# Performance work log

Hardware: AMD Instinct MI355X
Metric: run time of the kernel (lower is better)

The kernel has to match this reference:

```python
import jax, jax.numpy as jnp
import numpy as np
import math

B, C, BINS, W = 2, 8, 1024, 512
HEADS = 16
HD = BINS // HEADS          # 64 head dim
ROT = BINS // HEADS // 2    # 32 rotated dims
EXP = 4
EPS = 1e-5
MAX_FREQ = 10.0


def setup_inputs() -> dict:
    key = jax.random.key(0)
    ks = jax.random.split(key, 8)
    def u(k, shape, fan_in):
        lim = 1.0 / math.sqrt(fan_in)
        return jax.random.uniform(k, shape, jnp.float32, -lim, lim)
    return {
        "x": jax.random.normal(ks[0], (B, C, BINS, W), jnp.float32),
        "norm1_w": jnp.ones((BINS,), jnp.float32),
        "norm1_b": jnp.zeros((BINS,), jnp.float32),
        # 'pixel' rotary init: linspace(1, max_freq/2, dim//2) * pi (learned)
        "rot_freqs": jnp.linspace(1.0, MAX_FREQ / 2, ROT // 2, dtype=jnp.float32) * math.pi,
        "q_w": u(ks[1], (C, BINS, BINS), BINS),
        "out_w": u(ks[2], (C, BINS, BINS), BINS),
        "norm2_w": jnp.ones((BINS,), jnp.float32),
        "norm2_b": jnp.zeros((BINS,), jnp.float32),
        "lin1_w": u(ks[3], (C, BINS * EXP, BINS), BINS),
        "lin2_w": u(ks[4], (C, BINS, BINS * EXP), BINS * EXP),
    }


def _mlin(x, w):
    # x: [b,c,f_in,w]; w: [c,f_out,f_in] -> [b,c,f_out,w]
    return jnp.einsum('bcfw,cgf->bcgw', x, w)


def _frame_norm(x, w, b):
    # LayerNorm over the bins axis (axis=2) of [b,c,bins,w]
    m = jnp.mean(x, axis=2, keepdims=True)
    v = jnp.var(x, axis=2, keepdims=True)
    xn = (x - m) * jax.lax.rsqrt(v + EPS)
    return xn * w[:, None] + b[:, None]


def _rotate(q, cos, sin):
    # q: [b,c,h,w,d]; rotate first ROT dims with interleaved-pair rotate_half
    q1, q2 = q[..., :ROT], q[..., ROT:]
    qp = q1.reshape(*q1.shape[:-1], ROT // 2, 2)
    rh = jnp.stack([-qp[..., 1], qp[..., 0]], axis=-1).reshape(q1.shape)
    return jnp.concatenate([q1 * cos + rh * sin, q2], axis=-1)


def _attention(x, rot_freqs, q_w, out_w):
    b, c, bins, w = x.shape
    # faithful to source: q, k, v ALL use q_proj
    y = _mlin(x, q_w)  # [b,c,bins,w]
    # -> [b,c,h,w,d]
    y = y.transpose(0, 1, 3, 2).reshape(b, c, w, HEADS, HD).transpose(0, 1, 3, 2, 4)
    # rotary angles: t * freqs, repeat-interleaved x2 -> [w, ROT]
    t = jnp.arange(w, dtype=jnp.float32)
    ang = jnp.repeat(t[:, None] * rot_freqs[None, :], 2, axis=-1)
    cos, sin = jnp.cos(ang), jnp.sin(ang)
    q = _rotate(y, cos, sin)
    k = _rotate(y, cos, sin)
    v = y
    # NOTE: source scales by 1/sqrt(h) where h == bins (spectral height)
    scores = jnp.einsum('bchwd,bchud->bchwu', q, k) / math.sqrt(bins)
    a = jnp.einsum('bchwu,bchud->bchwd', jax.nn.softmax(scores, axis=-1), v)
    # [b,c,h,w,d] -> [b,c,bins,w]
    a = a.transpose(0, 1, 3, 2, 4).reshape(b, c, w, bins).transpose(0, 1, 3, 2)
    return _mlin(a, out_w)


def reference(x, norm1_w, norm1_b, rot_freqs, q_w, out_w,
              norm2_w, norm2_b, lin1_w, lin2_w):
    z = _frame_norm(x, norm1_w, norm1_b)
    z = _attention(z, rot_freqs, q_w, out_w)
    x = x + z  # dropout=0 -> identity
    z = _frame_norm(x, norm2_w, norm2_b)
    z = _mlin(jax.nn.gelu(_mlin(z, lin1_w), approximate=False), lin2_w)
    return x + z
```

## Files before the change

### kernel.cpp

```cpp
#include <hip/hip_runtime.h>
#include <math.h>

#define BB 2
#define CCH 8
#define BINS 1024
#define WW 512
#define HEADS 16
#define HD 64
#define ROTD 32
#define EXPF 4
#define NXE 8388608L
#define NTW 32

typedef unsigned short ushortT;
typedef short bf16x8 __attribute__((ext_vector_type(8)));
typedef float f32x4 __attribute__((ext_vector_type(4)));

__device__ __forceinline__ ushortT f2bf(float f) {
    unsigned int u = __float_as_uint(f);
    u = (u + 0x7FFF + ((u >> 16) & 1)) >> 16;
    return (ushortT)u;
}
__device__ __forceinline__ float bf2f(ushortT h) {
    return __uint_as_float(((unsigned int)h) << 16);
}
__device__ __forceinline__ float geluf(float x) {
    return 0.5f * x * (1.f + erff(x * 0.70710678118654752f));
}
__device__ __forceinline__ void gl_lds16(const ushortT* g, ushortT* l) {
    __builtin_amdgcn_global_load_lds(
        (const __attribute__((address_space(1))) unsigned int*)g,
        (__attribute__((address_space(3))) unsigned int*)l, 16, 0, 0);
}

__global__ __launch_bounds__(256)
void wcast_k(const float* __restrict__ s, ushortT* __restrict__ d, long n)
{
    long i = ((long)blockIdx.x * 256 + threadIdx.x) * 8;
    if (i >= n) return;
    float4 a = *(const float4*)&s[i];
    float4 b = *(const float4*)&s[i + 4];
    union { ushortT h[8]; uint4 v; } r;
    r.h[0] = f2bf(a.x); r.h[1] = f2bf(a.y); r.h[2] = f2bf(a.z); r.h[3] = f2bf(a.w);
    r.h[4] = f2bf(b.x); r.h[5] = f2bf(b.y); r.h[6] = f2bf(b.z); r.h[7] = f2bf(b.w);
    *(uint4*)&d[i] = r.v;
}

__global__ __launch_bounds__(1024)
void normT_k(const float* __restrict__ X, const float* __restrict__ wgt,
             const float* __restrict__ bia, ushortT* __restrict__ YT)
{
    __shared__ float tile[NTW][BINS + 1];
    __shared__ float red0[32][NTW], red1[32][NTW];
    __shared__ float ms[NTW], is[NTW];
    const int bc = blockIdx.x >> 4;
    const int w0 = (blockIdx.x & 15) * NTW;
    const int tid = threadIdx.x;
    const int w  = tid & (NTW - 1);
    const int fy = tid >> 5;
    const float* Xb = X + (long)bc * BINS * WW + w0;
    float s = 0.f, s2 = 0.f;
    for (int f = fy; f < BINS; f += 32) {
        float v = Xb[(long)f * WW + w];
        s += v; s2 += v * v;
        tile[w][f] = v;
    }
    red0[fy][w] = s; red1[fy][w] = s2;
    __syncthreads();
    if (tid < NTW) {
        float ss = 0.f, qq = 0.f;
        #pragma unroll
        for (int j = 0; j < 32; ++j) { ss += red0[j][tid]; qq += red1[j][tid]; }
        float m = ss * (1.f / BINS);
        float var = qq * (1.f / BINS) - m * m;
        ms[tid] = m; is[tid] = rsqrtf(var + 1e-5f);
    }
    __syncthreads();
    const int w2 = tid >> 5;
    const int c  = tid & 31;
    float m = ms[w2], inv = is[w2];
    ushortT* Yb = YT + ((long)bc * WW + w0 + w2) * BINS;
    #pragma unroll
    for (int jj = 0; jj < 4; ++jj) {
        int f0 = jj * 256 + c * 8;
        union { ushortT h[8]; uint4 v; } r;
        #pragma unroll
        for (int e = 0; e < 8; ++e) {
            int f = f0 + e;
            float v = (tile[w2][f] - m) * inv * wgt[f] + bia[f];
            r.h[e] = f2bf(v);
        }
        *(uint4*)&Yb[f0] = r.v;
    }
}

__global__ void rope_tab_k(const float* __restrict__ freqs,
                           float* __restrict__ cosT, float* __restrict__ sinT)
{
    int idx = blockIdx.x * 256 + threadIdx.x;
    if (idx >= WW * 16) return;
    int w = idx >> 4, i = idx & 15;
    float ang = (float)w * freqs[i];
    cosT[idx] = cosf(ang);
    sinT[idx] = sinf(ang);
}

__global__ __launch_bounds__(256)
void ropeB_k(const ushortT* __restrict__ yT, const float* __restrict__ cosT,
             const float* __restrict__ sinT, ushortT* __restrict__ rotT)
{
    long e0 = ((long)blockIdx.x * 256 + threadIdx.x) * 8;
    if (e0 >= NXE) return;
    int g0 = (int)(e0 & 1023);
    int w  = (int)((e0 >> 10) & 511);
    int d0 = g0 & 63;
    union { uint4 v; ushortT h8[8]; } in, ov;
    in.v = *(const uint4*)&yT[e0];
    if (d0 >= ROTD) {
        *(uint4*)&rotT[e0] = in.v;
        return;
    }
    #pragma unroll
    for (int j = 0; j < 8; j += 2) {
        int i = (d0 + j) >> 1;
        float c = cosT[w * 16 + i], s = sinT[w * 16 + i];
        float a = bf2f(in.h8[j]), b = bf2f(in.h8[j + 1]);
        ov.h8[j]     = f2bf(a * c - b * s);
        ov.h8[j + 1] = f2bf(b * c + a * s);
    }
    *(uint4*)&rotT[e0] = ov.v;
}

__global__ __launch_bounds__(256)
void mattn_k(const ushortT* __restrict__ rotT, const ushortT* __restrict__ yT,
             ushortT* __restrict__ oT)
{
    __shared__ ushortT Qs[64 * 64];
    __shared__ ushortT Ks[64 * 64];
    __shared__ ushortT Vs[64 * 72];
    __shared__ ushortT Ps[64 * 72];
    const int z = blockIdx.y;
    const int bc = z >> 4, h = z & 15;
    const int wq0 = blockIdx.x * 64;
    const int tid = threadIdx.x;
    const int wv = tid >> 6, l = tid & 63;
    const int lr = l & 15, lk = l >> 4;
    const long hbase = (long)bc * WW * 1024 + h * 64;

    #pragma unroll
    for (int p = 0; p < 2; ++p) {
        int r0 = p * 32 + wv * 8;
        int row = r0 + (l >> 3);
        int gs = (l & 7) ^ (row & 7);
        gl_lds16(rotT + hbase + (long)(wq0 + row) * 1024 + gs * 8, Qs + r0 * 64);
    }

    f32x4 oacc[4] = {};
    float mrow[4] = {-INFINITY, -INFINITY, -INFINITY, -INFINITY};
    float lrow[4] = {0.f, 0.f, 0.f, 0.f};

    for (int u0 = 0; u0 < WW; u0 += 64) {
        #pragma unroll
        for (int p = 0; p < 2; ++p) {
            int r0 = p * 32 + wv * 8;
            int row = r0 + (l >> 3);
            int gs = (l & 7) ^ (row & 7);
            gl_lds16(rotT + hbase + (long)(u0 + row) * 1024 + gs * 8, Ks + r0 * 64);
        }
        #pragma unroll
        for (int rep = 0; rep < 2; ++rep) {
            int ch = rep * 4 + wv;
            union { uint4 v; ushortT h8[8]; } tmp;
            tmp.v = *(const uint4*)(yT + hbase + (long)(u0 + l) * 1024 + ch * 8);
            #pragma unroll
            for (int j = 0; j < 8; ++j)
                Vs[(ch * 8 + j) * 72 + l] = tmp.h8[j];
        }
        __syncthreads();

        f32x4 sacc[4] = {};
        #pragma unroll
        for (int ko = 0; ko < 2; ++ko) {
            int ar = wv * 16 + lr;
            bf16x8 aq = *(const bf16x8*)&Qs[ar * 64 + (((ko * 4) + lk) ^ (ar & 7)) * 8];
            #pragma unroll
            for (int f = 0; f < 4; ++f) {
                int br = f * 16 + lr;
                bf16x8 bk = *(const bf16x8*)&Ks[br * 64 + (((ko * 4) + lk) ^ (br & 7)) * 8];
                sacc[f] = __builtin_amdgcn_mfma_f32_16x16x32_bf16(aq, bk, sacc[f], 0, 0, 0);
            }
        }

        #pragma unroll
        for (int rg = 0; rg < 4; ++rg) {
            float s0 = sacc[0][rg] * (1.f / 32.f);
            float s1 = sacc[1][rg] * (1.f / 32.f);
            float s2 = sacc[2][rg] * (1.f / 32.f);
            float s3 = sacc[3][rg] * (1.f / 32.f);
            float mx = fmaxf(fmaxf(s0, s1), fmaxf(s2, s3));
            mx = fmaxf(mx, __shfl_xor(mx, 1));
            mx = fmaxf(mx, __shfl_xor(mx, 2));
            mx = fmaxf(mx, __shfl_xor(mx, 4));
            mx = fmaxf(mx, __shfl_xor(mx, 8));
            float mnew = fmaxf(mrow[rg], mx);
            float al = __expf(mrow[rg] - mnew);
            float p0 = __expf(s0 - mnew), p1 = __expf(s1 - mnew);
            float p2 = __expf(s2 - mnew), p3 = __expf(s3 - mnew);
            float rs = p0 + p1 + p2 + p3;
            rs += __shfl_xor(rs, 1);
            rs += __shfl_xor(rs, 2);
            rs += __shfl_xor(rs, 4);
            rs += __shfl_xor(rs, 8);
            lrow[rg] = lrow[rg] * al + rs;
            mrow[rg] = mnew;
            oacc[0][rg] *= al; oacc[1][rg] *= al;
            oacc[2][rg] *= al; oacc[3][rg] *= al;
            int prow = wv * 16 + lk * 4 + rg;
            Ps[prow * 72 +  0 + lr] = f2bf(p0);
            Ps[prow * 72 + 16 + lr] = f2bf(p1);
            Ps[prow * 72 + 32 + lr] = f2bf(p2);
            Ps[prow * 72 + 48 + lr] = f2bf(p3);
        }
        asm volatile("s_waitcnt lgkmcnt(0)" ::: "memory");

        #pragma unroll
        for (int ko = 0; ko < 2; ++ko) {
            int ar = wv * 16 + lr;
            bf16x8 ap = *(const bf16x8*)&Ps[ar * 72 + ko * 32 + lk * 8];
            #pragma unroll
            for (int f = 0; f < 4; ++f) {
                bf16x8 bv = *(const bf16x8*)&Vs[(f * 16 + lr) * 72 + ko * 32 + lk * 8];
                oacc[f] = __builtin_amdgcn_mfma_f32_16x16x32_bf16(ap, bv, oacc[f], 0, 0, 0);
            }
        }
        __syncthreads();
    }

    #pragma unroll
    for (int rg = 0; rg < 4; ++rg) {
        float inv = 1.f / lrow[rg];
        int w = wq0 + wv * 16 + lk * 4 + rg;
        long b2 = (long)bc * WW * 1024 + (long)w * 1024 + h * 64;
        #pragma unroll
        for (int f = 0; f < 4; ++f)
            oT[b2 + f * 16 + lr] = f2bf(oacc[f][rg] * inv);
    }
}

template<bool HASRES, bool GELUF, bool TRANSOUT>
__global__ __launch_bounds__(256)
void mgemm_k(const ushortT* __restrict__ A, long sA, int aMod,
             const ushortT* __restrict__ B, long sB,
             void* __restrict__ Cp, long sC,
             const float* __restrict__ R, long sR,
             int M, int N, int K)
{
    __shared__ ushortT smem[(128 + 128) * 64];
    ushortT* As = smem;
    ushortT* Bs = smem + 128 * 64;
    const int z = blockIdx.z;
    const ushortT* Ab = A + (long)(z % aMod) * sA + (long)blockIdx.y * 128 * K;
    const ushortT* Bb = B + (long)z * sB + (long)blockIdx.x * 128 * K;
    const int tid = threadIdx.x;
    const int wv = tid >> 6, l = tid & 63;
    const int lrow = l & 15, lk = l >> 4;
    const int mb = (wv >> 1) * 64, nb = (wv & 1) * 64;
    f32x4 acc[4][4] = {};

    for (int k0 = 0; k0 < K; k0 += 64) {
        #pragma unroll
        for (int t = 0; t < 4; ++t) {
            int r0 = wv * 32 + t * 8;
            int row = r0 + (l >> 3);
            int gs = (l & 7) ^ (row & 7);
            gl_lds16(Ab + (long)row * K + k0 + gs * 8, As + r0 * 64);
            gl_lds16(Bb + (long)row * K + k0 + gs * 8, Bs + r0 * 64);
        }
        __syncthreads();
        #pragma unroll
        for (int ko = 0; ko < 2; ++ko) {
            bf16x8 af[4], bg[4];
            #pragma unroll
            for (int i = 0; i < 4; ++i) {
                int ra = mb + i * 16 + lrow;
                af[i] = *(const bf16x8*)&As[ra * 64 + ((lk + ko * 4) ^ (ra & 7)) * 8];
                int rb = nb + i * 16 + lrow;
                bg[i] = *(const bf16x8*)&Bs[rb * 64 + ((lk + ko * 4) ^ (rb & 7)) * 8];
            }
            #pragma unroll
            for (int i = 0; i < 4; ++i)
                #pragma unroll
                for (int j = 0; j < 4; ++j)
                    acc[i][j] = __builtin_amdgcn_mfma_f32_16x16x32_bf16(
                        af[i], bg[j], acc[i][j], 0, 0, 0);
        }
        __syncthreads();
    }

    const int m0g = blockIdx.y * 128 + mb, n0g = blockIdx.x * 128 + nb;
    if (!TRANSOUT) {
        float* Cf = (float*)Cp + (long)z * sC;
        #pragma unroll
        for (int i = 0; i < 4; ++i)
            #pragma unroll
            for (int j = 0; j < 4; ++j)
                #pragma unroll
                for (int rg = 0; rg < 4; ++rg) {
                    long m = m0g + i * 16 + lk * 4 + rg;
                    long n = n0g + j * 16 + lrow;
                    float v = acc[i][j][rg];
                    if (GELUF) v = geluf(v);
                    if (HASRES) v += R[(long)z * sR + m * N + n];
                    Cf[m * N + n] = v;
                }
    } else {
        ushortT* Ts = smem + wv * 4096;
        #pragma unroll
        for (int i = 0; i < 4; ++i)
            #pragma unroll
            for (int j = 0; j < 4; ++j)
                #pragma unroll
                for (int rg = 0; rg < 4; ++rg) {
                    int ml = i * 16 + lk * 4 + rg;
                    int nl = j * 16 + lrow;
                    float v = acc[i][j][rg];
                    if (GELUF) v = geluf(v);
                    Ts[nl * 64 + (((ml >> 3) ^ (nl & 7)) << 3) + (ml & 7)] = f2bf(v);
                }
        __syncthreads();
        ushortT* CT = (ushortT*)Cp + (long)z * sC;
        #pragma unroll
        for (int p = 0; p < 8; ++p) {
            int nl = p * 8 + (l >> 3), mc = l & 7;
            uint4 d = *(const uint4*)&Ts[nl * 64 + ((mc ^ (nl & 7)) << 3)];
            *(uint4*)&CT[(long)(n0g + nl) * M + m0g + mc * 8] = d;
        }
    }
}

extern "C" void kernel_launch(void* const* d_in, const int* in_sizes, int n_in,
                              void* d_out, int out_size, void* d_ws, size_t ws_size,
                              hipStream_t stream)
{
    const float* x    = (const float*)d_in[0];
    const float* n1w  = (const float*)d_in[1];
    const float* n1b  = (const float*)d_in[2];
    const float* freqs= (const float*)d_in[3];
    const float* qw   = (const float*)d_in[4];
    const float* ow   = (const float*)d_in[5];
    const float* n2w  = (const float*)d_in[6];
    const float* n2b  = (const float*)d_in[7];
    const float* l1w  = (const float*)d_in[8];
    const float* l2w  = (const float*)d_in[9];
    float* out = (float*)d_out;
    char* wsb  = (char*)d_ws;
    const long MB = 1L << 20;

    ushortT* qwB  = (ushortT*)(wsb +   0 * MB);
    ushortT* owB  = (ushortT*)(wsb +  16 * MB);
    ushortT* znT  = (ushortT*)(wsb +  32 * MB);
    ushortT* CfT  = (ushortT*)(wsb +  32 * MB);
    ushortT* l1wB = (ushortT*)(wsb +   0 * MB);
    ushortT* l2wB = (ushortT*)(wsb +   0 * MB);
    ushortT* yT   = (ushortT*)(wsb +  64 * MB);
    ushortT* zn2T = (ushortT*)(wsb +  64 * MB);
    ushortT* rotT = (ushortT*)(wsb +  80 * MB);
    ushortT* h1T  = (ushortT*)(wsb +  96 * MB);
    float*   cosT = (float*)  (wsb + 160 * MB);
    float*   sinT = cosT + WW * 16;

    rope_tab_k<<<32, 256, 0, stream>>>(freqs, cosT, sinT);

    wcast_k<<<4096, 256, 0, stream>>>(qw, qwB, 8L * BINS * BINS);
    wcast_k<<<4096, 256, 0, stream>>>(ow, owB, 8L * BINS * BINS);

    normT_k<<<BB * CCH * 16, 1024, 0, stream>>>(x, n1w, n1b, znT);

    mgemm_k<false, false, true><<<dim3(4, 8, 16), 256, 0, stream>>>(
        qwB, (long)BINS * BINS, CCH,
        znT, (long)WW * BINS,
        yT,  (long)WW * BINS,
        nullptr, 0, BINS, WW, BINS);

    ropeB_k<<<4096, 256, 0, stream>>>(yT, cosT, sinT, rotT);

    mattn_k<<<dim3(8, 256), 256, 0, stream>>>(rotT, yT, CfT);

    mgemm_k<true, false, false><<<dim3(4, 8, 16), 256, 0, stream>>>(
        owB, (long)BINS * BINS, CCH,
        CfT, (long)WW * BINS,
        out, (long)BINS * WW,
        x,   (long)BINS * WW, BINS, WW, BINS);

    wcast_k<<<16384, 256, 0, stream>>>(l1w, l1wB, 8L * BINS * EXPF * BINS);

    normT_k<<<BB * CCH * 16, 1024, 0, stream>>>(out, n2w, n2b, zn2T);

    mgemm_k<false, true, true><<<dim3(4, 32, 16), 256, 0, stream>>>(
        l1wB, (long)BINS * EXPF * BINS, CCH,
        zn2T, (long)WW * BINS,
        h1T,  (long)WW * BINS * EXPF,
        nullptr, 0, BINS * EXPF, WW, BINS);

    wcast_k<<<16384, 256, 0, stream>>>(l2w, l2wB, 8L * BINS * EXPF * BINS);

    mgemm_k<true, false, false><<<dim3(4, 8, 16), 256, 0, stream>>>(
        l2wB, (long)BINS * BINS * EXPF, CCH,
        h1T,  (long)WW * BINS * EXPF,
        out,  (long)BINS * WW,
        out,  (long)BINS * WW, BINS, WW, BINS * EXPF);
}
```

Measured before the change: 477.1 us.

## Fuse fp32-to-bf16 weight cast into double-buffered GEMM with XCD-aware block remap

Removes the separate weight-cast kernels. The GEMM now loads fp32 weights straight into registers, converts them to bf16 and writes them into LDS, so the extra write and re-read of the bf16 weight copies goes away. The GEMM main loop becomes double-buffered, prefetching the next K tile while the current one computes. A 1D grid is remapped so consecutive logical tiles spread across the 8 XCDs. In exchange, weight reads from global memory are twice as wide, and register pressure and LDS use (64KB) rise, which may lower occupancy.

```diff
diff --git a/kernel.cpp b/kernel.cpp
--- a/kernel.cpp
+++ b/kernel.cpp
@@ -31,19 +31,6 @@
     __builtin_amdgcn_global_load_lds(
         (const __attribute__((address_space(1))) unsigned int*)g,
         (__attribute__((address_space(3))) unsigned int*)l, 16, 0, 0);
-}
-
-__global__ __launch_bounds__(256)
-void wcast_k(const float* __restrict__ s, ushortT* __restrict__ d, long n)
-{
-    long i = ((long)blockIdx.x * 256 + threadIdx.x) * 8;
-    if (i >= n) return;
-    float4 a = *(const float4*)&s[i];
-    float4 b = *(const float4*)&s[i + 4];
-    union { ushortT h[8]; uint4 v; } r;
-    r.h[0] = f2bf(a.x); r.h[1] = f2bf(a.y); r.h[2] = f2bf(a.z); r.h[3] = f2bf(a.w);
-    r.h[4] = f2bf(b.x); r.h[5] = f2bf(b.y); r.h[6] = f2bf(b.z); r.h[7] = f2bf(b.w);
-    *(uint4*)&d[i] = r.v;
 }
 
 __global__ __launch_bounds__(1024)
@@ -249,43 +236,77 @@
 
 template<bool HASRES, bool GELUF, bool TRANSOUT>
 __global__ __launch_bounds__(256)
-void mgemm_k(const ushortT* __restrict__ A, long sA, int aMod,
+void fgemm_k(const float* __restrict__ A, long sA, int aMod,
              const ushortT* __restrict__ B, long sB,
              void* __restrict__ Cp, long sC,
              const float* __restrict__ R, long sR,
-             int M, int N, int K)
-{
-    __shared__ ushortT smem[(128 + 128) * 64];
-    ushortT* As = smem;
-    ushortT* Bs = smem + 128 * 64;
-    const int z = blockIdx.z;
-    const ushortT* Ab = A + (long)(z % aMod) * sA + (long)blockIdx.y * 128 * K;
-    const ushortT* Bb = B + (long)z * sB + (long)blockIdx.x * 128 * K;
+             int M, int N, int K, int gx, int gy)
+{
+    __shared__ ushortT smem[4 * 8192];
+    const int nwg = gridDim.x;
+    const int bid = blockIdx.x;
+    const int lid = (bid & 7) * (nwg >> 3) + (bid >> 3);
+    const int x = lid % gx;
+    const int y = (lid / gx) % gy;
+    const int z = lid / (gx * gy);
+    const float*   Ab = A + (long)(z % aMod) * sA + (long)y * 128 * K;
+    const ushortT* Bb = B + (long)z * sB + (long)x * 128 * K;
     const int tid = threadIdx.x;
     const int wv = tid >> 6, l = tid & 63;
     const int lrow = l & 15, lk = l >> 4;
     const int mb = (wv >> 1) * 64, nb = (wv & 1) * 64;
+    const int ar0 = tid >> 3 << 0;
     f32x4 acc[4][4] = {};
-
-    for (int k0 = 0; k0 < K; k0 += 64) {
+    float4 a0[4], a1[4];
+
+    const int NT = K >> 6;
+
+    auto fetchA = [&](int k0) {
+        #pragma unroll
+        for (int c = 0; c < 4; ++c) {
+            int idx = tid + c * 256;
+            int row = idx >> 3, grp = idx & 7;
+            const float* src = Ab + (long)row * K + k0 + grp * 8;
+            a0[c] = *(const float4*)src;
+            a1[c] = *(const float4*)(src + 4);
+        }
+    };
+    auto commitA = [&](int buf) {
+        ushortT* AsB = smem + buf * 16384;
+        #pragma unroll
+        for (int c = 0; c < 4; ++c) {
+            int idx = tid + c * 256;
+            int row = idx >> 3, grp = idx & 7;
+            union { ushortT h[8]; uint4 v; } r;
+            r.h[0] = f2bf(a0[c].x); r.h[1] = f2bf(a0[c].y);
+            r.h[2] = f2bf(a0[c].z); r.h[3] = f2bf(a0[c].w);
+            r.h[4] = f2bf(a1[c].x); r.h[5] = f2bf(a1[c].y);
+            r.h[6] = f2bf(a1[c].z); r.h[7] = f2bf(a1[c].w);
+            *(uint4*)&AsB[row * 64 + ((grp ^ (row & 7)) << 3)] = r.v;
+        }
+    };
+    auto stageB = [&](int buf, int k0) {
+        ushortT* BsB = smem + 8192 + buf * 16384;
         #pragma unroll
         for (int t = 0; t < 4; ++t) {
             int r0 = wv * 32 + t * 8;
             int row = r0 + (l >> 3);
             int gs = (l & 7) ^ (row & 7);
-            gl_lds16(Ab + (long)row * K + k0 + gs * 8, As + r0 * 64);
-            gl_lds16(Bb + (long)row * K + k0 + gs * 8, Bs + r0 * 64);
-        }
-        __syncthreads();
+            gl_lds16(Bb + (long)row * K + k0 + gs * 8, BsB + r0 * 64);
+        }
+    };
+    auto compute = [&](int buf) {
+        const ushortT* AsB = smem + buf * 16384;
+        const ushortT* BsB = smem + 8192 + buf * 16384;
         #pragma unroll
         for (int ko = 0; ko < 2; ++ko) {
             bf16x8 af[4], bg[4];
             #pragma unroll
             for (int i = 0; i < 4; ++i) {
                 int ra = mb + i * 16 + lrow;
-                af[i] = *(const bf16x8*)&As[ra * 64 + ((lk + ko * 4) ^ (ra & 7)) * 8];
+                af[i] = *(const bf16x8*)&AsB[ra * 64 + ((lk + ko * 4) ^ (ra & 7)) * 8];
                 int rb = nb + i * 16 + lrow;
-                bg[i] = *(const bf16x8*)&Bs[rb * 64 + ((lk + ko * 4) ^ (rb & 7)) * 8];
+                bg[i] = *(const bf16x8*)&BsB[rb * 64 + ((lk + ko * 4) ^ (rb & 7)) * 8];
             }
             #pragma unroll
             for (int i = 0; i < 4; ++i)
@@ -294,10 +315,26 @@
                     acc[i][j] = __builtin_amdgcn_mfma_f32_16x16x32_bf16(
                         af[i], bg[j], acc[i][j], 0, 0, 0);
         }
+    };
+
+    fetchA(0);
+    stageB(0, 0);
+    commitA(0);
+    asm volatile("s_waitcnt vmcnt(0) lgkmcnt(0)" ::: "memory");
+    __syncthreads();
+
+    for (int t = 0; t < NT; ++t) {
+        int buf = t & 1;
+        if (t + 1 < NT) { fetchA((t + 1) << 6); stageB(buf ^ 1, (t + 1) << 6); }
+        compute(buf);
+        if (t + 1 < NT) {
+            commitA(buf ^ 1);
+            asm volatile("s_waitcnt vmcnt(0) lgkmcnt(0)" ::: "memory");
+        }
         __syncthreads();
     }
 
-    const int m0g = blockIdx.y * 128 + mb, n0g = blockIdx.x * 128 + nb;
+    const int m0g = y * 128 + mb, n0g = x * 128 + nb;
     if (!TRANSOUT) {
         float* Cf = (float*)Cp + (long)z * sC;
         #pragma unroll
@@ -315,6 +352,7 @@
                 }
     } else {
         ushortT* Ts = smem + wv * 4096;
+        __syncthreads();
         #pragma unroll
         for (int i = 0; i < 4; ++i)
             #pragma unroll
@@ -356,57 +394,46 @@
     char* wsb  = (char*)d_ws;
     const long MB = 1L << 20;
 
-    ushortT* qwB  = (ushortT*)(wsb +   0 * MB);
-    ushortT* owB  = (ushortT*)(wsb +  16 * MB);
-    ushortT* znT  = (ushortT*)(wsb +  32 * MB);
-    ushortT* CfT  = (ushortT*)(wsb +  32 * MB);
-    ushortT* l1wB = (ushortT*)(wsb +   0 * MB);
-    ushortT* l2wB = (ushortT*)(wsb +   0 * MB);
-    ushortT* yT   = (ushortT*)(wsb +  64 * MB);
+    ushortT* znT  = (ushortT*)(wsb +   0 * MB);
+    ushortT* yT   = (ushortT*)(wsb +  16 * MB);
+    ushortT* rotT = (ushortT*)(wsb +  32 * MB);
+    ushortT* CfT  = (ushortT*)(wsb +  48 * MB);
     ushortT* zn2T = (ushortT*)(wsb +  64 * MB);
-    ushortT* rotT = (ushortT*)(wsb +  80 * MB);
-    ushortT* h1T  = (ushortT*)(wsb +  96 * MB);
-    float*   cosT = (float*)  (wsb + 160 * MB);
+    ushortT* h1T  = (ushortT*)(wsb +  80 * MB);
+    float*   cosT = (float*)  (wsb + 144 * MB);
     float*   sinT = cosT + WW * 16;
 
     rope_tab_k<<<32, 256, 0, stream>>>(freqs, cosT, sinT);
 
-    wcast_k<<<4096, 256, 0, stream>>>(qw, qwB, 8L * BINS * BINS);
-    wcast_k<<<4096, 256, 0, stream>>>(ow, owB, 8L * BINS * BINS);
-
     normT_k<<<BB * CCH * 16, 1024, 0, stream>>>(x, n1w, n1b, znT);
 
-    mgemm_k<false, false, true><<<dim3(4, 8, 16), 256, 0, stream>>>(
-        qwB, (long)BINS * BINS, CCH,
+    fgemm_k<false, false, true><<<512, 256, 0, stream>>>(
+        qw,  (long)BINS * BINS, CCH,
         znT, (long)WW * BINS,
         yT,  (long)WW * BINS,
-        nullptr, 0, BINS, WW, BINS);
+        nullptr, 0, BINS, WW, BINS, 4, 8);
 
     ropeB_k<<<4096, 256, 0, stream>>>(yT, cosT, sinT, rotT);
 
     mattn_k<<<dim3(8, 256), 256, 0, stream>>>(rotT, yT, CfT);
 
-    mgemm_k<true, false, false><<<dim3(4, 8, 16), 256, 0, stream>>>(
-        owB, (long)BINS * BINS, CCH,
+    fgemm_k<true, false, false><<<512, 256, 0, stream>>>(
+        ow,  (long)BINS * BINS, CCH,
         CfT, (long)WW * BINS,
         out, (long)BINS * WW,
-        x,   (long)BINS * WW, BINS, WW, BINS);
-
-    wcast_k<<<16384, 256, 0, stream>>>(l1w, l1wB, 8L * BINS * EXPF * BINS);
+        x,   (long)BINS * WW, BINS, WW, BINS, 4, 8);
 
     normT_k<<<BB * CCH * 16, 1024, 0, stream>>>(out, n2w, n2b, zn2T);
 
-    mgemm_k<false, true, true><<<dim3(4, 32, 16), 256, 0, stream>>>(
-        l1wB, (long)BINS * EXPF * BINS, CCH,
+    fgemm_k<false, true, true><<<2048, 256, 0, stream>>>(
+        l1w,  (long)BINS * EXPF * BINS, CCH,
         zn2T, (long)WW * BINS,
         h1T,  (long)WW * BINS * EXPF,
-        nullptr, 0, BINS * EXPF, WW, BINS);
-
-    wcast_k<<<16384, 256, 0, stream>>>(l2w, l2wB, 8L * BINS * EXPF * BINS);
-
-    mgemm_k<true, false, false><<<dim3(4, 8, 16), 256, 0, stream>>>(
-        l2wB, (long)BINS * BINS * EXPF, CCH,
-        h1T,  (long)WW * BINS * EXPF,
-        out,  (long)BINS * WW,
-        out,  (long)BINS * WW, BINS, WW, BINS * EXPF);
-}
+        nullptr, 0, BINS * EXPF, WW, BINS, 4, 32);
+
+    fgemm_k<true, false, false><<<512, 256, 0, stream>>>(
+        l2w, (long)BINS * BINS * EXPF, CCH,
+        h1T, (long)WW * BINS * EXPF,
+        out, (long)BINS * WW,
+        out, (long)BINS * WW, BINS, WW, BINS * EXPF, 4, 8);
+}
```

New measurement: 457.7 us. -4.1%, faster.
